# Performance work log

Measured on AMD Instinct MI355X. Metric: run time of the kernel, lower is better.

The kernel has to match this reference:

```python
import jax, jax.numpy as jnp
import numpy as np

NUM_HEADS = 48
EMBED_DIM = 768


def setup_inputs() -> dict:
    key = jax.random.key(0)
    ks = jax.random.split(key, 12)
    b, n, e, n_exp = 2, 512, EMBED_DIM, 256
    m = n + n_exp  # expanded kv length (periodic images appended)
    s = 0.02
    return {
        "query": jax.random.normal(ks[0], (b, n, e), jnp.float32),
        "attn_bias": jax.random.normal(ks[1], (b * NUM_HEADS, n, m), jnp.float32),
        "delta_pos": jax.random.normal(ks[2], (b, n, m, 3), jnp.float32),
        "outcell_index": jax.random.randint(ks[3], (b, n_exp), 0, n, jnp.int32),
        "Wq": jax.random.normal(ks[4], (e, e), jnp.float32) * s,
        "bq": jnp.zeros((e,), jnp.float32),
        "Wk": jax.random.normal(ks[5], (e, e), jnp.float32) * s,
        "bk": jnp.zeros((e,), jnp.float32),
        "Wv": jax.random.normal(ks[6], (e, e), jnp.float32) * s,
        "bv": jnp.zeros((e,), jnp.float32),
        "w_force": jax.random.normal(ks[7], (e,), jnp.float32) * s,
    }


def reference(query, attn_bias, delta_pos, outcell_index, Wq, bq, Wk, bk, Wv, bv, w_force):
    b, n, e = query.shape
    H = NUM_HEADS
    d = e // H
    scaling = d ** (-0.5)

    def proj(W, bias):
        # [b, n, e] -> [b, H, n, d]
        return (query @ W.T + bias).reshape(b, n, H, d).transpose(0, 2, 1, 3)

    q = proj(Wq, bq) * scaling
    k = proj(Wk, bk)
    v = proj(Wv, bv)

    # periodic-image KV expansion: gather nodes along axis 2, concat
    idx = outcell_index[:, None, :, None]  # [b, 1, n_exp, 1] broadcasts over H, d
    k = jnp.concatenate([k, jnp.take_along_axis(k, idx, axis=2)], axis=2)
    v = jnp.concatenate([v, jnp.take_along_axis(v, idx, axis=2)], axis=2)
    m = k.shape[2]  # n_node_expand

    attn = jnp.einsum('bhnd,bhmd->bhnm', q, k)
    probs = jax.nn.softmax(attn + attn_bias.reshape(b, H, n, m), axis=-1)
    # dropout p=0.1 is identity in eval mode

    # position-weighted value aggregation: [b,h,n,m]*[b,n,m,3] contracted with v over m
    x = jnp.einsum('bhnm,bnmc,bhmd->bnchd', probs, delta_pos, v).reshape(b, n, 3, e)
    force = jnp.einsum('bnce,e->bnc', x, w_force).astype(jnp.float32)  # [b, n, 3]
    return force
```

## Files before the change

kernel.cpp:

```cpp
#include <hip/hip_runtime.h>
#include <cstdint>
#include <cstddef>

#define BDIM 2
#define NQ 512
#define NEXP 256
#define MDIM 768
#define HN 48
#define DD 16
#define ED 768

typedef short v8s __attribute__((ext_vector_type(8)));
typedef float v4f __attribute__((ext_vector_type(4)));

__global__ void prep_kernel(const float* __restrict__ Wv, const float* __restrict__ bv,
                            const float* __restrict__ wf,
                            float* __restrict__ wve, float* __restrict__ ube) {
  int h = blockIdx.x;
  float wl[DD];
#pragma unroll
  for (int d = 0; d < DD; ++d) wl[d] = wf[h * DD + d];
  for (int k = threadIdx.x; k < ED; k += blockDim.x) {
    float s = 0.f;
#pragma unroll
    for (int d = 0; d < DD; ++d) s = fmaf(wl[d], Wv[(size_t)(h * DD + d) * ED + k], s);
    wve[(size_t)h * ED + k] = s;
  }
  if (threadIdx.x == 0) {
    float s = 0.f;
#pragma unroll
    for (int d = 0; d < DD; ++d) s = fmaf(wl[d], bv[h * DD + d], s);
    ube[h] = s;
  }
}

__global__ __launch_bounds__(256) void convert_kernel(
    const float* __restrict__ query, const float* __restrict__ Wq,
    const float* __restrict__ Wk, const float* __restrict__ wve,
    ushort* __restrict__ Abf, ushort* __restrict__ Bbf) {
  const int id = blockIdx.x * 256 + threadIdx.x;
  const float* src = nullptr;
  ushort* dst;
  if (id < 98304) {
    const int off = id * 8;
    src = query + off;
    dst = Abf + off;
  } else {
    const int id2 = id - 98304;
    const int r = id2 / 96;
    const int k = (id2 - r * 96) * 8;
    dst = Bbf + (size_t)r * 768 + k;
    if (r < 768)       src = Wq + (size_t)r * 768 + k;
    else if (r < 1536) src = Wk + (size_t)(r - 768) * 768 + k;
    else if (r < 1584) src = wve + (size_t)(r - 1536) * 768 + k;
  }
  union { ushort s[8]; uint4 v; } p;
  if (src) {
    const float4 v0 = *(const float4*)src;
    const float4 v1 = *(const float4*)(src + 4);
    const float vv[8] = {v0.x, v0.y, v0.z, v0.w, v1.x, v1.y, v1.z, v1.w};
#pragma unroll
    for (int i = 0; i < 8; ++i) {
      union { float f; uint32_t u; } c; c.f = vv[i];
      p.s[i] = (ushort)((c.u + 0x7FFFu + ((c.u >> 16) & 1u)) >> 16);
    }
  } else {
#pragma unroll
    for (int i = 0; i < 8; ++i) p.s[i] = 0;
  }
  *(uint4*)dst = p.v;
}

__global__ __launch_bounds__(256) void proj_mfma(
    const ushort* __restrict__ Abf, const ushort* __restrict__ Bbf,
    const float* __restrict__ bq, const float* __restrict__ bk,
    const float* __restrict__ ube,
    float* __restrict__ qs, float* __restrict__ ke, float* __restrict__ ub) {
  __shared__ __align__(16) ushort As[4][4][16][8];
  __shared__ __align__(16) ushort Bs[4][64][8];
  const int tid = threadIdx.x;
  const int wave = tid >> 6, lane = tid & 63;
  const int m0 = blockIdx.y * 64, n0 = blockIdx.x * 64;
  const int arow = tid >> 2;
  const int aseg = tid & 3;
  v4f acc[4] = {v4f{0,0,0,0}, v4f{0,0,0,0}, v4f{0,0,0,0}, v4f{0,0,0,0}};

  for (int k0 = 0; k0 < ED; k0 += 32) {
    __syncthreads();
    *(uint4*)&As[arow >> 4][aseg][arow & 15][0] =
        *(const uint4*)&Abf[(size_t)(m0 + arow) * ED + k0 + aseg * 8];
    *(uint4*)&Bs[aseg][arow][0] =
        *(const uint4*)&Bbf[(size_t)(n0 + arow) * ED + k0 + aseg * 8];
    __syncthreads();
    const v8s af = *(const v8s*)&As[wave][lane >> 4][lane & 15][0];
#pragma unroll
    for (int nt = 0; nt < 4; ++nt) {
      const v8s bfr = *(const v8s*)&Bs[lane >> 4][nt * 16 + (lane & 15)][0];
      acc[nt] = __builtin_amdgcn_mfma_f32_16x16x32_bf16(af, bfr, acc[nt], 0, 0, 0);
    }
  }

#pragma unroll
  for (int nt = 0; nt < 4; ++nt) {
    const int c = n0 + nt * 16 + (lane & 15);
    if (c >= 1584) continue;
#pragma unroll
    for (int r = 0; r < 4; ++r) {
      const int row = m0 + wave * 16 + (lane >> 4) * 4 + r;
      const int b = row >> 9, n = row & 511;
      const float val = acc[nt][r];
      if (c < 768) {
        qs[(size_t)(b * NQ + n) * ED + c] = (val + bq[c]) * 0.25f;
      } else if (c < 1536) {
        const int ck = c - 768;
        const int hh = ck >> 4, dd = ck & 15;
        ke[(size_t)((b * HN + hh) * DD + dd) * MDIM + n] = val + bk[ck];
      } else {
        const int hh = c - 1536;
        ub[(size_t)(b * HN + hh) * MDIM + n] = val + ube[hh];
      }
    }
  }
}

__global__ void gather_kernel(const int* __restrict__ idx, float* __restrict__ ke,
                              float* __restrict__ ub) {
  const int id = blockIdx.x * 256 + threadIdx.x;
  const int N1 = BDIM * HN * DD * NEXP;
  if (id < N1) {
    int j = id & (NEXP - 1);
    int d = (id >> 8) & (DD - 1);
    int hb = id >> 12;
    int n = idx[(hb / HN) * NEXP + j];
    float* row = ke + (size_t)(hb * DD + d) * MDIM;
    row[NQ + j] = row[n];
  } else {
    int id2 = id - N1;
    if (id2 < BDIM * HN * NEXP) {
      int j = id2 & (NEXP - 1);
      int hb = id2 >> 8;
      int n = idx[(hb / HN) * NEXP + j];
      float* row = ub + (size_t)hb * MDIM;
      row[NQ + j] = row[n];
    }
  }
}

__device__ __forceinline__ void fma4(float4& a, float q, const float4& k) {
  a.x = fmaf(q, k.x, a.x); a.y = fmaf(q, k.y, a.y);
  a.z = fmaf(q, k.z, a.z); a.w = fmaf(q, k.w, a.w);
}

__global__ __launch_bounds__(256) void fused_kernel(
    const float* __restrict__ qs, const float* __restrict__ ke, const float* __restrict__ ub,
    const float* __restrict__ bias, float* __restrict__ Wp) {
  __shared__ __align__(16) float Ks[DD * MDIM];
  const int bid = blockIdx.x;
  const int b = bid & 1;
  const int hg = (bid >> 1) & 3;
  const int n0 = (bid >> 3) * 4;
  const int wave = threadIdx.x >> 6;
  const int lane = threadIdx.x & 63;
  const int r = n0 + wave;
  const int hbase = hg * 12;

  float4 wacc[3] = {};
  float4 a[3];

  {
    const float4* bp = (const float4*)(bias + (size_t)((b * HN + hbase) * NQ + r) * MDIM);
#pragma unroll
    for (int j = 0; j < 3; ++j) a[j] = bp[lane + 64 * j];
  }

  for (int hi = 0; hi < 12; ++hi) {
    const int h = hbase + hi;

    __syncthreads();
    {
      const float4* src = (const float4*)(ke + (size_t)(b * HN + h) * DD * MDIM);
      float4* dst = (float4*)Ks;
#pragma unroll
      for (int it = 0; it < 12; ++it)
        dst[it * 256 + threadIdx.x] = src[it * 256 + threadIdx.x];
    }
    __syncthreads();

    const float4* u4 = (const float4*)(ub + (size_t)(b * HN + h) * MDIM);
    const float4 u0 = u4[lane], u1 = u4[lane + 64], u2 = u4[lane + 128];

    const float4* qp4 = (const float4*)(qs + (size_t)(b * NQ + r) * ED + h * DD);
    const float4 q0 = qp4[0], q1 = qp4[1], q2 = qp4[2], q3 = qp4[3];

    const float4* kl = (const float4*)Ks;
#pragma unroll
    for (int d4 = 0; d4 < 4; ++d4) {
      const float4 qv = (d4 == 0) ? q0 : (d4 == 1) ? q1 : (d4 == 2) ? q2 : q3;
#pragma unroll
      for (int dd = 0; dd < 4; ++dd) {
        const int d = d4 * 4 + dd;
        const float4 k0 = kl[d * 192 + lane];
        const float4 k1 = kl[d * 192 + lane + 64];
        const float4 k2 = kl[d * 192 + lane + 128];
        const float qd = (dd == 0) ? qv.x : (dd == 1) ? qv.y : (dd == 2) ? qv.z : qv.w;
        fma4(a[0], qd, k0);
        fma4(a[1], qd, k1);
        fma4(a[2], qd, k2);
      }
    }

    float mx = -1e30f;
#pragma unroll
    for (int j = 0; j < 3; ++j)
      mx = fmaxf(mx, fmaxf(fmaxf(a[j].x, a[j].y), fmaxf(a[j].z, a[j].w)));
#pragma unroll
    for (int sh = 32; sh > 0; sh >>= 1) mx = fmaxf(mx, __shfl_xor(mx, sh));
    float e[12];
#pragma unroll
    for (int j = 0; j < 3; ++j) {
      e[j * 4 + 0] = __expf(a[j].x - mx);
      e[j * 4 + 1] = __expf(a[j].y - mx);
      e[j * 4 + 2] = __expf(a[j].z - mx);
      e[j * 4 + 3] = __expf(a[j].w - mx);
    }
    if (hi < 11) {
      const float4* bp = (const float4*)(bias + (size_t)((b * HN + h + 1) * NQ + r) * MDIM);
#pragma unroll
      for (int j = 0; j < 3; ++j) a[j] = bp[lane + 64 * j];
    }
    float l = 0.f;
#pragma unroll
    for (int k = 0; k < 12; ++k) l += e[k];
#pragma unroll
    for (int sh = 32; sh > 0; sh >>= 1) l += __shfl_xor(l, sh);
    const float inv = 1.0f / l;
#pragma unroll
    for (int j = 0; j < 3; ++j) {
      const float4 uu = (j == 0) ? u0 : (j == 1) ? u1 : u2;
      wacc[j].x = fmaf(e[j * 4 + 0] * inv, uu.x, wacc[j].x);
      wacc[j].y = fmaf(e[j * 4 + 1] * inv, uu.y, wacc[j].y);
      wacc[j].z = fmaf(e[j * 4 + 2] * inv, uu.z, wacc[j].z);
      wacc[j].w = fmaf(e[j * 4 + 3] * inv, uu.w, wacc[j].w);
    }
  }

  float4* wp = (float4*)Wp;
#pragma unroll
  for (int j = 0; j < 3; ++j)
    wp[((size_t)(b * NQ + r) * 4 + hg) * 192 + lane + 64 * j] = wacc[j];
}

__global__ __launch_bounds__(256) void force_kernel(
    const float* __restrict__ Wp, const float* __restrict__ dp, float* __restrict__ out) {
  const int wave = threadIdx.x >> 6;
  const int lane = threadIdx.x & 63;
  const int row = blockIdx.x * 4 + wave;
  const float4* wp = (const float4*)Wp;
  float4 ws[3];
#pragma unroll
  for (int j = 0; j < 3; ++j) {
    float4 s = wp[((size_t)row * 4 + 0) * 192 + lane + 64 * j];
#pragma unroll
    for (int hg = 1; hg < 4; ++hg) {
      const float4 t = wp[((size_t)row * 4 + hg) * 192 + lane + 64 * j];
      s.x += t.x; s.y += t.y; s.z += t.z; s.w += t.w;
    }
    ws[j] = s;
  }
  const float* dpp = dp + (size_t)row * MDIM * 3;
  float f0 = 0.f, f1 = 0.f, f2 = 0.f;
#pragma unroll
  for (int j = 0; j < 3; ++j) {
    const float4 w = ws[j];
    const int m0 = j * 256 + lane * 4;
    const float4* dv = (const float4*)(dpp + (size_t)m0 * 3);
    const float4 d0 = dv[0], d1 = dv[1], d2 = dv[2];
    f0 = fmaf(w.x, d0.x, f0); f0 = fmaf(w.y, d0.w, f0); f0 = fmaf(w.z, d1.z, f0); f0 = fmaf(w.w, d2.y, f0);
    f1 = fmaf(w.x, d0.y, f1); f1 = fmaf(w.y, d1.x, f1); f1 = fmaf(w.z, d1.w, f1); f1 = fmaf(w.w, d2.z, f1);
    f2 = fmaf(w.x, d0.z, f2); f2 = fmaf(w.y, d1.y, f2); f2 = fmaf(w.z, d2.x, f2); f2 = fmaf(w.w, d2.w, f2);
  }
#pragma unroll
  for (int sh = 32; sh > 0; sh >>= 1) {
    f0 += __shfl_xor(f0, sh);
    f1 += __shfl_xor(f1, sh);
    f2 += __shfl_xor(f2, sh);
  }
  if (lane == 0) {
    float* op = out + (size_t)row * 3;
    op[0] = f0; op[1] = f1; op[2] = f2;
  }
}

extern "C" void kernel_launch(void* const* d_in, const int* in_sizes, int n_in,
                              void* d_out, int out_size, void* d_ws, size_t ws_size,
                              hipStream_t stream) {
  const float* query     = (const float*)d_in[0];
  const float* attn_bias = (const float*)d_in[1];
  const float* delta_pos = (const float*)d_in[2];
  const int*   outcell   = (const int*)d_in[3];
  const float* Wq = (const float*)d_in[4];
  const float* bq = (const float*)d_in[5];
  const float* Wk = (const float*)d_in[6];
  const float* bk = (const float*)d_in[7];
  const float* Wv = (const float*)d_in[8];
  const float* bv = (const float*)d_in[9];
  const float* wf = (const float*)d_in[10];
  float* out = (float*)d_out;
  float* ws  = (float*)d_ws;

  float* wve  = ws;
  float* ube  = ws + 36864;
  float* qsb  = ws + 36928;
  float* keb  = ws + 823360;
  float* ubb  = ws + 2003008;
  float* Wpb  = ws + 2076736;
  ushort* Abf = (ushort*)(ws + 5222464);
  ushort* Bbf = (ushort*)(ws + 5615680);

  prep_kernel<<<HN, 256, 0, stream>>>(Wv, bv, wf, wve, ube);
  convert_kernel<<<984, 256, 0, stream>>>(query, Wq, Wk, wve, Abf, Bbf);
  proj_mfma<<<dim3(25, 16), 256, 0, stream>>>(Abf, Bbf, bq, bk, ube, qsb, keb, ubb);
  gather_kernel<<<1632, 256, 0, stream>>>(outcell, keb, ubb);
  fused_kernel<<<1024, 256, 0, stream>>>(qsb, keb, ubb, attn_bias, Wpb);
  force_kernel<<<256, 256, 0, stream>>>(Wpb, delta_pos, out);
}
```

Baseline: 295.4 us.

## Stage K tiles via direct global-to-LDS loads in halves, reduce LDS

Replaces the register-staged copy of each head's K block into shared memory with global_load_lds direct-to-LDS transfers. The K block is now loaded in two 8-row halves, which halves the LDS footprint to 24KB so more blocks can be resident per CU. The exp values reuse the score registers, and the next head's bias prefetch moves after the weighted accumulation. The cost is twice as many barriers per head and a later bias prefetch, which gives less latency hiding for that load.

```diff
diff --git a/kernel.cpp b/kernel.cpp
--- a/kernel.cpp
+++ b/kernel.cpp
@@ -151,10 +151,16 @@
   a.z = fmaf(q, k.z, a.z); a.w = fmaf(q, k.w, a.w);
 }
 
+__device__ __forceinline__ void gload_lds16(const float4* g, float4* l) {
+  __builtin_amdgcn_global_load_lds(
+      (const __attribute__((address_space(1))) void*)g,
+      (__attribute__((address_space(3))) void*)l, 16, 0, 0);
+}
+
 __global__ __launch_bounds__(256) void fused_kernel(
     const float* __restrict__ qs, const float* __restrict__ ke, const float* __restrict__ ub,
     const float* __restrict__ bias, float* __restrict__ Wp) {
-  __shared__ __align__(16) float Ks[DD * MDIM];
+  __shared__ __align__(16) float Ks[8 * MDIM];
   const int bid = blockIdx.x;
   const int b = bid & 1;
   const int hg = (bid >> 1) & 3;
@@ -175,72 +181,76 @@
 
   for (int hi = 0; hi < 12; ++hi) {
     const int h = hbase + hi;
-
-    __syncthreads();
-    {
-      const float4* src = (const float4*)(ke + (size_t)(b * HN + h) * DD * MDIM);
-      float4* dst = (float4*)Ks;
-#pragma unroll
-      for (int it = 0; it < 12; ++it)
-        dst[it * 256 + threadIdx.x] = src[it * 256 + threadIdx.x];
-    }
-    __syncthreads();
+    const float4* qp4 = (const float4*)(qs + (size_t)(b * NQ + r) * ED + h * DD);
+    const float4* kl = (const float4*)Ks;
+
+#pragma unroll
+    for (int dh = 0; dh < 2; ++dh) {
+      __syncthreads();
+      {
+        const float4* src = (const float4*)(ke + ((size_t)(b * HN + h) * DD + dh * 8) * MDIM);
+        float4* dstb = (float4*)Ks;
+#pragma unroll
+        for (int it = 0; it < 6; ++it) {
+          const int base = (it * 4 + wave) * 64;
+          gload_lds16(src + base + lane, dstb + base);
+        }
+      }
+      __syncthreads();
+
+      const float4 q0 = qp4[dh * 2], q1 = qp4[dh * 2 + 1];
+#pragma unroll
+      for (int d4 = 0; d4 < 2; ++d4) {
+        const float4 qv = d4 ? q1 : q0;
+#pragma unroll
+        for (int dd = 0; dd < 4; ++dd) {
+          const int d = d4 * 4 + dd;
+          const float4 k0 = kl[d * 192 + lane];
+          const float4 k1 = kl[d * 192 + lane + 64];
+          const float4 k2 = kl[d * 192 + lane + 128];
+          const float qd = (dd == 0) ? qv.x : (dd == 1) ? qv.y : (dd == 2) ? qv.z : qv.w;
+          fma4(a[0], qd, k0);
+          fma4(a[1], qd, k1);
+          fma4(a[2], qd, k2);
+        }
+      }
+    }
 
     const float4* u4 = (const float4*)(ub + (size_t)(b * HN + h) * MDIM);
     const float4 u0 = u4[lane], u1 = u4[lane + 64], u2 = u4[lane + 128];
 
-    const float4* qp4 = (const float4*)(qs + (size_t)(b * NQ + r) * ED + h * DD);
-    const float4 q0 = qp4[0], q1 = qp4[1], q2 = qp4[2], q3 = qp4[3];
-
-    const float4* kl = (const float4*)Ks;
-#pragma unroll
-    for (int d4 = 0; d4 < 4; ++d4) {
-      const float4 qv = (d4 == 0) ? q0 : (d4 == 1) ? q1 : (d4 == 2) ? q2 : q3;
-#pragma unroll
-      for (int dd = 0; dd < 4; ++dd) {
-        const int d = d4 * 4 + dd;
-        const float4 k0 = kl[d * 192 + lane];
-        const float4 k1 = kl[d * 192 + lane + 64];
-        const float4 k2 = kl[d * 192 + lane + 128];
-        const float qd = (dd == 0) ? qv.x : (dd == 1) ? qv.y : (dd == 2) ? qv.z : qv.w;
-        fma4(a[0], qd, k0);
-        fma4(a[1], qd, k1);
-        fma4(a[2], qd, k2);
-      }
-    }
-
     float mx = -1e30f;
 #pragma unroll
     for (int j = 0; j < 3; ++j)
       mx = fmaxf(mx, fmaxf(fmaxf(a[j].x, a[j].y), fmaxf(a[j].z, a[j].w)));
 #pragma unroll
     for (int sh = 32; sh > 0; sh >>= 1) mx = fmaxf(mx, __shfl_xor(mx, sh));
-    float e[12];
 #pragma unroll
     for (int j = 0; j < 3; ++j) {
-      e[j * 4 + 0] = __expf(a[j].x - mx);
-      e[j * 4 + 1] = __expf(a[j].y - mx);
-      e[j * 4 + 2] = __expf(a[j].z - mx);
-      e[j * 4 + 3] = __expf(a[j].w - mx);
-    }
+      a[j].x = __expf(a[j].x - mx);
+      a[j].y = __expf(a[j].y - mx);
+      a[j].z = __expf(a[j].z - mx);
+      a[j].w = __expf(a[j].w - mx);
+    }
+    float l = 0.f;
+#pragma unroll
+    for (int j = 0; j < 3; ++j) { l += a[j].x; l += a[j].y; l += a[j].z; l += a[j].w; }
+#pragma unroll
+    for (int sh = 32; sh > 0; sh >>= 1) l += __shfl_xor(l, sh);
+    const float inv = 1.0f / l;
+#pragma unroll
+    for (int j = 0; j < 3; ++j) {
+      const float4 uu = (j == 0) ? u0 : (j == 1) ? u1 : u2;
+      wacc[j].x = fmaf(a[j].x * inv, uu.x, wacc[j].x);
+      wacc[j].y = fmaf(a[j].y * inv, uu.y, wacc[j].y);
+      wacc[j].z = fmaf(a[j].z * inv, uu.z, wacc[j].z);
+      wacc[j].w = fmaf(a[j].w * inv, uu.w, wacc[j].w);
+    }
+
     if (hi < 11) {
       const float4* bp = (const float4*)(bias + (size_t)((b * HN + h + 1) * NQ + r) * MDIM);
 #pragma unroll
       for (int j = 0; j < 3; ++j) a[j] = bp[lane + 64 * j];
-    }
-    float l = 0.f;
-#pragma unroll
-    for (int k = 0; k < 12; ++k) l += e[k];
-#pragma unroll
-    for (int sh = 32; sh > 0; sh >>= 1) l += __shfl_xor(l, sh);
-    const float inv = 1.0f / l;
-#pragma unroll
-    for (int j = 0; j < 3; ++j) {
-      const float4 uu = (j == 0) ? u0 : (j == 1) ? u1 : u2;
-      wacc[j].x = fmaf(e[j * 4 + 0] * inv, uu.x, wacc[j].x);
-      wacc[j].y = fmaf(e[j * 4 + 1] * inv, uu.y, wacc[j].y);
-      wacc[j].z = fmaf(e[j * 4 + 2] * inv, uu.z, wacc[j].z);
-      wacc[j].w = fmaf(e[j * 4 + 3] * inv, uu.w, wacc[j].w);
     }
   }
 
```

Result: no change. 292.9 us (-0.8%).
